# Performance work log

Hardware: AMD Instinct MI355X
Metric: run time of the kernel (lower is better)

The kernel has to match this reference:

```python
import jax, jax.numpy as jnp
import numpy as np

B, L, H = 2, 2048, 1024
NH = 4
K = int(H * 0.5)       # key_dim = 512
V = int(H * 1.0)       # value_dim = 1024
DK, DV = K // NH, V // NH   # 128, 256
PR = 32                # proj_low_rank_dim
GR = 64                # gate_low_rank_dim
EPS = 1e-5


def setup_inputs() -> dict:
    key = jax.random.key(0)
    ks = jax.random.split(key, 16)
    s = 0.02
    return {
        "x": jax.random.normal(ks[0], (B, L, H), jnp.float32),
        "mu_x": jax.random.normal(ks[1], (H,), jnp.float32) * s,      # LerpLinear mu of x_proj[0]
        "Wx1": jax.random.normal(ks[2], (5 * PR, H), jnp.float32) * s,  # x_proj[0].linear
        "Wx2": jax.random.normal(ks[3], (H, 5 * PR), jnp.float32) * s,  # x_proj[2]
        "x_bias": jax.random.normal(ks[4], (5, H), jnp.float32) * s,
        "Wr": jax.random.normal(ks[5], (K, H), jnp.float32) * s,
        "Wk": jax.random.normal(ks[6], (K, H), jnp.float32) * s,
        "Wv": jax.random.normal(ks[7], (V, H), jnp.float32) * s,
        "Wg": jax.random.normal(ks[8], (V, H), jnp.float32) * s,
        "Ww1": jax.random.normal(ks[9], (GR, H), jnp.float32) * s,     # w_proj LoRA down
        "Ww2": jax.random.normal(ks[10], (K, GR), jnp.float32) * s,    # w_proj LoRA up
        "bw2": jax.random.normal(ks[11], (K,), jnp.float32) * s,
        "bonus": jax.random.normal(ks[12], (NH, DK), jnp.float32) * s,  # u
        "ln_w": jnp.ones((DV,), jnp.float32),
        "ln_b": jnp.zeros((DV,), jnp.float32),
        "Wo": jax.random.normal(ks[13], (H, V), jnp.float32) * s,
    }


def reference(x, mu_x, Wx1, Wx2, x_bias, Wr, Wk, Wv, Wg, Ww1, Ww2, bw2,
              bonus, ln_w, ln_b, Wo):
    b, l, h = x.shape
    # token shift: shifted[t] = x[t-1], zeros at t=0 (nn.ZeroPad2d((0,0,1,-1)))
    shifted = jnp.pad(x, ((0, 0), (1, 0), (0, 0)))[:, :-1]
    delta = shifted - x

    # x_proj: LerpLinear -> tanh -> einsum with o_proj-like weight, 5 mixing vectors
    xp = jnp.tanh((x + delta * mu_x) @ Wx1.T).reshape(b, l, 5, PR)
    mus = jnp.einsum('blnr,hnr->blnh', xp, Wx2.reshape(H, 5, PR)) + x_bias
    mu_r, mu_w, mu_k, mu_v, mu_g = (mus[:, :, i] for i in range(5))

    # DDLerpLinear projections: linear(x + delta * mu)
    r = (x + delta * mu_r) @ Wr.T                                   # [B,L,K]
    w = jnp.tanh((x + delta * mu_w) @ Ww1.T) @ Ww2.T + bw2          # LoRA, [B,L,K]
    k = (x + delta * mu_k) @ Wk.T                                   # [B,L,K]
    v = (x + delta * mu_v) @ Wv.T                                   # [B,L,V]
    g = (x + delta * mu_g) @ Wg.T                                   # [B,L,V]

    r = r.reshape(b, l, NH, DK)
    k = k.reshape(b, l, NH, DK)
    v = v.reshape(b, l, NH, DV)
    w = -jnp.exp(w.reshape(b, l, NH, DK))   # log-decay (negative)

    def step(S, inp):
        r_t, k_t, v_t, w_t = inp                                    # [B,h,dk]/[B,h,dv]
        kv = k_t[..., :, None] * v_t[..., None, :]                  # [B,h,dk,dv]
        o_t = jnp.einsum('bhk,bhkv->bhv', r_t,
                         S + bonus[None, :, :, None] * kv)
        S = jnp.exp(w_t)[..., None] * S + kv
        return S, o_t

    seq = (r.transpose(1, 0, 2, 3), k.transpose(1, 0, 2, 3),
           v.transpose(1, 0, 2, 3), w.transpose(1, 0, 2, 3))
    S0 = jnp.zeros((b, NH, DK, DV), x.dtype)
    _, o = jax.lax.scan(step, S0, seq)       # [L,B,h,dv]
    o = o.transpose(1, 0, 2, 3)              # [B,L,h,dv]

    # per-head LayerNorm fused with swish gate
    mean = o.mean(-1, keepdims=True)
    var = o.var(-1, keepdims=True)
    o = (o - mean) * jax.lax.rsqrt(var + EPS) * ln_w + ln_b
    gh = g.reshape(b, l, NH, DV)
    o = o * (gh * jax.nn.sigmoid(gh))        # swish gate

    return o.reshape(b, l, V) @ Wo.T         # [B,L,H]
```

## Files before the change

kernel.cpp:

```cpp
#include <hip/hip_runtime.h>
#include <cstdint>
#include <cstddef>

#define H     1024
#define LSEQ  2048
#define NHH   4
#define DKK   128
#define DVV   256
#define KDIM  512
#define VDIM  1024
#define GRR   64
#define MTOT  4096

enum { EPI_NONE = 0, EPI_TANH = 1, EPI_DEC = 3 };

typedef __attribute__((ext_vector_type(8))) _Float16 half8;
typedef __attribute__((ext_vector_type(4))) float f32x4;
typedef __attribute__((ext_vector_type(2))) float f32x2;

static __device__ __forceinline__ unsigned short f2h(float f) {
    _Float16 h = (_Float16)f;
    union { _Float16 h; unsigned short u; } c;
    c.h = h;
    return c.u;
}

static __device__ __forceinline__ f32x2 pk_fma(f32x2 a, f32x2 b, f32x2 c) {
    return __builtin_elementwise_fma(a, b, c);
}
static __device__ __forceinline__ f32x2 bcast2(float s) {
    f32x2 r; r.x = s; r.y = s; return r;
}

template<int CTRL>
static __device__ __forceinline__ f32x2 dpp_add2(f32x2 x) {
    int lo = __builtin_amdgcn_update_dpp(0, __float_as_int(x.x), CTRL, 0xf, 0xf, true);
    int hi = __builtin_amdgcn_update_dpp(0, __float_as_int(x.y), CTRL, 0xf, 0xf, true);
    f32x2 m;
    m.x = __int_as_float(lo);
    m.y = __int_as_float(hi);
    return x + m;
}

__global__ __launch_bounds__(256) void lerp5_kernel(
    const float* __restrict__ xp,
    const float* __restrict__ Wx2,
    const float* __restrict__ xb,
    const float* __restrict__ x,
    unsigned short* __restrict__ insb)
{
    __shared__ float As[16][64];
    __shared__ float Bs[16][64];
    const int m0 = blockIdx.x * 64;
    const int n0 = blockIdx.y * 64;
    const int t  = threadIdx.x;
    const int tx = t & 15, ty = t >> 4;
    const int sm = t >> 2;
    const int sq = (t & 3) * 4;
    const int nbase = n0 + tx * 4;

    float4 xv[4], pv[4];
#pragma unroll
    for (int i = 0; i < 4; i++) {
        const int m = m0 + ty * 4 + i;
        xv[i] = *(const float4*)(x + (size_t)m * H + nbase);
        pv[i] = make_float4(0.f, 0.f, 0.f, 0.f);
        if ((m & (LSEQ - 1)) != 0)
            pv[i] = *(const float4*)(x + (size_t)(m - 1) * H + nbase);
    }

    for (int z = 0; z < 5; z++) {
        const int acol = z * 32;
        float acc[4][4];
#pragma unroll
        for (int i = 0; i < 4; i++)
#pragma unroll
            for (int j = 0; j < 4; j++) acc[i][j] = 0.f;

#pragma unroll
        for (int k0 = 0; k0 < 32; k0 += 16) {
            {
                const int m = m0 + sm;
                const float4 av = *(const float4*)(xp + (size_t)m * 256 + acol + k0 + sq);
                As[sq + 0][sm] = av.x; As[sq + 1][sm] = av.y;
                As[sq + 2][sm] = av.z; As[sq + 3][sm] = av.w;
            }
            {
                const int n = n0 + sm;
                const float4 bv = *(const float4*)(Wx2 + (size_t)n * 160 + acol + k0 + sq);
                Bs[sq + 0][sm] = bv.x; Bs[sq + 1][sm] = bv.y;
                Bs[sq + 2][sm] = bv.z; Bs[sq + 3][sm] = bv.w;
            }
            __syncthreads();
#pragma unroll
            for (int kk = 0; kk < 16; kk++) {
                const float4 a = *(const float4*)&As[kk][ty * 4];
                const float4 b = *(const float4*)&Bs[kk][tx * 4];
                const float av2[4] = {a.x, a.y, a.z, a.w};
                const float bv2[4] = {b.x, b.y, b.z, b.w};
#pragma unroll
                for (int i = 0; i < 4; i++)
#pragma unroll
                    for (int j = 0; j < 4; j++) acc[i][j] += av2[i] * bv2[j];
            }
            __syncthreads();
        }

        const float4 bb = *(const float4*)(xb + z * H + nbase);
        unsigned short* dst = insb + (size_t)z * 4194304;
#pragma unroll
        for (int i = 0; i < 4; i++) {
            const int m = m0 + ty * 4 + i;
            float4 r;
            r.x = xv[i].x + (pv[i].x - xv[i].x) * (acc[i][0] + bb.x);
            r.y = xv[i].y + (pv[i].y - xv[i].y) * (acc[i][1] + bb.y);
            r.z = xv[i].z + (pv[i].z - xv[i].z) * (acc[i][2] + bb.z);
            r.w = xv[i].w + (pv[i].w - xv[i].w) * (acc[i][3] + bb.w);
            ushort4 p;
            p.x = f2h(r.x); p.y = f2h(r.y); p.z = f2h(r.z); p.w = f2h(r.w);
            *(ushort4*)(dst + (size_t)m * H + nbase) = p;
        }
    }
}

template<int EPI>
__global__ __launch_bounds__(256) void gemm_mfma_bt(
    const unsigned short* __restrict__ A,
    const unsigned short* __restrict__ A2, int nsplit, int lda,
    const unsigned short* __restrict__ B, int ldb,
    float* __restrict__ C, unsigned short* __restrict__ Ch, int ldc, int K,
    const float* __restrict__ bias)
{
    __shared__ __align__(16) unsigned short As[128 * 32];
    __shared__ __align__(16) unsigned short Bs[128 * 32];
    const int t    = threadIdx.x;
    const int w    = t >> 6;
    const int lane = t & 63;
    const int m0 = blockIdx.x * 128;
    const int n0 = blockIdx.y * 128;
    const unsigned short* Au = (n0 < nsplit) ? A : A2;
    const int mw = (w & 1) * 64;
    const int nw = (w >> 1) * 64;
    const int l15 = lane & 15;
    const int q4  = lane >> 4;

    f32x4 acc[4][4];
#pragma unroll
    for (int i = 0; i < 4; i++)
#pragma unroll
        for (int j = 0; j < 4; j++) {
            f32x4 z = {0.f, 0.f, 0.f, 0.f};
            acc[i][j] = z;
        }

    for (int k0 = 0; k0 < K; k0 += 32) {
        __syncthreads();
#pragma unroll
        for (int jj = 0; jj < 2; jj++) {
            const int c   = w * 128 + jj * 64 + lane;
            const int row = c >> 2;
            const int col = (c & 3) * 8;
            __builtin_amdgcn_global_load_lds(
                (const __attribute__((address_space(1))) void*)(Au + (size_t)(m0 + row) * lda + k0 + col),
                (__attribute__((address_space(3))) void*)((char*)As + (w * 128 + jj * 64) * 16),
                16, 0, 0);
            __builtin_amdgcn_global_load_lds(
                (const __attribute__((address_space(1))) void*)(B + (size_t)(n0 + row) * ldb + k0 + col),
                (__attribute__((address_space(3))) void*)((char*)Bs + (w * 128 + jj * 64) * 16),
                16, 0, 0);
        }
        __syncthreads();

        half8 a[4], b[4];
#pragma unroll
        for (int i = 0; i < 4; i++)
            a[i] = *(const half8*)(As + (mw + i * 16 + l15) * 32 + q4 * 8);
#pragma unroll
        for (int j = 0; j < 4; j++)
            b[j] = *(const half8*)(Bs + (nw + j * 16 + l15) * 32 + q4 * 8);
#pragma unroll
        for (int i = 0; i < 4; i++)
#pragma unroll
            for (int j = 0; j < 4; j++)
                acc[i][j] = __builtin_amdgcn_mfma_f32_16x16x32_f16(a[i], b[j], acc[i][j], 0, 0, 0);
    }

#pragma unroll
    for (int i = 0; i < 4; i++) {
        const int m_base = m0 + mw + i * 16 + q4 * 4;
#pragma unroll
        for (int j = 0; j < 4; j++) {
            const int n = n0 + nw + j * 16 + l15;
#pragma unroll
            for (int r = 0; r < 4; r++) {
                float val = acc[i][j][r];
                if constexpr (EPI == EPI_TANH) {
                    C[(size_t)(m_base + r) * ldc + n] = tanhf(val);
                } else if constexpr (EPI == EPI_DEC) {
                    C[(size_t)(m_base + r) * ldc + n] = expf(-expf(val + bias[n]));
                } else {
                    C[(size_t)(m_base + r) * ldc + n] = val;
                }
            }
        }
    }
}

__global__ __launch_bounds__(256) void gemm_fused3(
    const unsigned short* __restrict__ s0, const unsigned short* __restrict__ s1,
    const unsigned short* __restrict__ s2, const unsigned short* __restrict__ s3,
    const unsigned short* __restrict__ s4,
    const unsigned short* __restrict__ Ww1p, const unsigned short* __restrict__ Wrb,
    const unsigned short* __restrict__ Wvb,
    unsigned short* __restrict__ wlow16, float* __restrict__ rkB,
    float* __restrict__ vgB)
{
    const int y = blockIdx.y;
    const unsigned short *Au, *Bp;
    float* C = nullptr;
    unsigned short* Ch = nullptr;
    int n0, ldc;
    if (y == 0) {
        Au = s1; Bp = Ww1p; n0 = 0; ldc = 128; Ch = wlow16;
    } else if (y <= 8) {
        n0 = (y - 1) * 128;
        Au = (n0 < 512) ? s0 : s2;
        Bp = Wrb; C = rkB; ldc = 1024;
    } else {
        n0 = (y - 9) * 128;
        Au = (n0 < 1024) ? s3 : s4;
        Bp = Wvb; C = vgB; ldc = 2048;
    }

    __shared__ __align__(16) unsigned short As[128 * 32];
    __shared__ __align__(16) unsigned short Bs[128 * 32];
    const int t    = threadIdx.x;
    const int w    = t >> 6;
    const int lane = t & 63;
    const int m0 = blockIdx.x * 128;
    const int mw = (w & 1) * 64;
    const int nw = (w >> 1) * 64;
    const int l15 = lane & 15;
    const int q4  = lane >> 4;

    f32x4 acc[4][4];
#pragma unroll
    for (int i = 0; i < 4; i++)
#pragma unroll
        for (int j = 0; j < 4; j++) {
            f32x4 z = {0.f, 0.f, 0.f, 0.f};
            acc[i][j] = z;
        }

    for (int k0 = 0; k0 < H; k0 += 32) {
        __syncthreads();
#pragma unroll
        for (int jj = 0; jj < 2; jj++) {
            const int c   = w * 128 + jj * 64 + lane;
            const int row = c >> 2;
            const int col = (c & 3) * 8;
            __builtin_amdgcn_global_load_lds(
                (const __attribute__((address_space(1))) void*)(Au + (size_t)(m0 + row) * H + k0 + col),
                (__attribute__((address_space(3))) void*)((char*)As + (w * 128 + jj * 64) * 16),
                16, 0, 0);
            __builtin_amdgcn_global_load_lds(
                (const __attribute__((address_space(1))) void*)(Bp + (size_t)(n0 + row) * H + k0 + col),
                (__attribute__((address_space(3))) void*)((char*)Bs + (w * 128 + jj * 64) * 16),
                16, 0, 0);
        }
        __syncthreads();

        half8 a[4], b[4];
#pragma unroll
        for (int i = 0; i < 4; i++)
            a[i] = *(const half8*)(As + (mw + i * 16 + l15) * 32 + q4 * 8);
#pragma unroll
        for (int j = 0; j < 4; j++)
            b[j] = *(const half8*)(Bs + (nw + j * 16 + l15) * 32 + q4 * 8);
#pragma unroll
        for (int i = 0; i < 4; i++)
#pragma unroll
            for (int j = 0; j < 4; j++)
                acc[i][j] = __builtin_amdgcn_mfma_f32_16x16x32_f16(a[i], b[j], acc[i][j], 0, 0, 0);
    }

#pragma unroll
    for (int i = 0; i < 4; i++) {
        const int m_base = m0 + mw + i * 16 + q4 * 4;
#pragma unroll
        for (int j = 0; j < 4; j++) {
            const int n = n0 + nw + j * 16 + l15;
#pragma unroll
            for (int r = 0; r < 4; r++) {
                float val = acc[i][j][r];
                if (Ch) Ch[(size_t)(m_base + r) * ldc + n] = f2h(tanhf(val));
                else    C[(size_t)(m_base + r) * ldc + n] = val;
            }
        }
    }
}

__global__ __launch_bounds__(256) void gemm_mfma_corr(
    const unsigned short* __restrict__ rt16,
    const unsigned short* __restrict__ SentryT16,
    float* __restrict__ o, int segl)
{
    const int z   = blockIdx.z;
    const int seg = (z >> 3) + 1;
    const int bh  = z & 7;
    const int b   = bh >> 2, h = bh & 3;
    const unsigned short* A = rt16 + ((size_t)b * LSEQ + (size_t)seg * segl) * KDIM + h * DKK;
    const unsigned short* B = SentryT16 + (size_t)(seg * 8 + bh) * 32768;
    float* C = o + ((size_t)b * LSEQ + (size_t)seg * segl) * VDIM + h * DVV;

    __shared__ __align__(16) unsigned short As[128 * 32];
    __shared__ __align__(16) unsigned short Bs[128 * 32];
    const int t    = threadIdx.x;
    const int w    = t >> 6;
    const int lane = t & 63;
    const int m0 = blockIdx.x * 128;
    const int n0 = blockIdx.y * 128;
    const int mw = (w & 1) * 64;
    const int nw = (w >> 1) * 64;
    const int l15 = lane & 15;
    const int q4  = lane >> 4;

    f32x4 acc[4][4];
#pragma unroll
    for (int i = 0; i < 4; i++)
#pragma unroll
        for (int j = 0; j < 4; j++) {
            f32x4 zz = {0.f, 0.f, 0.f, 0.f};
            acc[i][j] = zz;
        }

    for (int k0 = 0; k0 < 128; k0 += 32) {
        __syncthreads();
#pragma unroll
        for (int jj = 0; jj < 2; jj++) {
            const int c   = w * 128 + jj * 64 + lane;
            const int row = c >> 2;
            const int col = (c & 3) * 8;
            __builtin_amdgcn_global_load_lds(
                (const __attribute__((address_space(1))) void*)(A + (size_t)(m0 + row) * KDIM + k0 + col),
                (__attribute__((address_space(3))) void*)((char*)As + (w * 128 + jj * 64) * 16),
                16, 0, 0);
            __builtin_amdgcn_global_load_lds(
                (const __attribute__((address_space(1))) void*)(B + (size_t)(n0 + row) * 128 + k0 + col),
                (__attribute__((address_space(3))) void*)((char*)Bs + (w * 128 + jj * 64) * 16),
                16, 0, 0);
        }
        __syncthreads();

        half8 a[4], bb[4];
#pragma unroll
        for (int i = 0; i < 4; i++)
            a[i] = *(const half8*)(As + (mw + i * 16 + l15) * 32 + q4 * 8);
#pragma unroll
        for (int j = 0; j < 4; j++)
            bb[j] = *(const half8*)(Bs + (nw + j * 16 + l15) * 32 + q4 * 8);
#pragma unroll
        for (int i = 0; i < 4; i++)
#pragma unroll
            for (int j = 0; j < 4; j++)
                acc[i][j] = __builtin_amdgcn_mfma_f32_16x16x32_f16(a[i], bb[j], acc[i][j], 0, 0, 0);
    }

#pragma unroll
    for (int i = 0; i < 4; i++) {
        const int mrow = mw + i * 16 + q4 * 4;
        const int m_base = m0 + mrow;
#pragma unroll
        for (int j = 0; j < 4; j++) {
            const int n = n0 + nw + j * 16 + l15;
#pragma unroll
            for (int rr = 0; rr < 4; rr++)
                if (mrow + rr < segl)
                    C[(size_t)(m_base + rr) * VDIM + n] += acc[i][j][rr];
        }
    }
}

__global__ __launch_bounds__(256) void prep_kernel(
    const float* __restrict__ Wr, const float* __restrict__ Wk,
    const float* __restrict__ Wv, const float* __restrict__ Wg,
    const float* __restrict__ Wo, const float* __restrict__ Wx1,
    const float* __restrict__ Ww1, const float* __restrict__ Ww2,
    unsigned short* __restrict__ Wb, unsigned short* __restrict__ Wx1p,
    unsigned short* __restrict__ Ww1p, unsigned short* __restrict__ Ww2p,
    const float* __restrict__ x, const float* __restrict__ mux,
    unsigned short* __restrict__ xl16)
{
    const int bx = blockIdx.x;
    if (bx < 4512) {
        const int q = bx * 256 + threadIdx.x;
        float4 v = make_float4(0.f, 0.f, 0.f, 0.f);
        unsigned short* dst;
        if (q < 1048576) {
            const int i4 = q * 4;
            const float* src; int off;
            if      (i4 <  524288) { src = Wr; off = i4; }
            else if (i4 < 1048576) { src = Wk; off = i4 -  524288; }
            else if (i4 < 2097152) { src = Wv; off = i4 - 1048576; }
            else if (i4 < 3145728) { src = Wg; off = i4 - 2097152; }
            else                   { src = Wo; off = i4 - 3145728; }
            v = *(const float4*)(src + off);
            dst = Wb + i4;
        } else if (q < 1114112) {
            const int e = (q - 1048576) * 4;
            const int row = e >> 10;
            if (row < 160) v = *(const float4*)(Wx1 + (size_t)row * H + (e & 1023));
            dst = Wx1p + e;
        } else if (q < 1146880) {
            const int e = (q - 1114112) * 4;
            const int row = e >> 10;
            if (row < 64) v = *(const float4*)(Ww1 + (size_t)row * H + (e & 1023));
            dst = Ww1p + e;
        } else {
            const int e = (q - 1146880) * 4;
            v = *(const float4*)(Ww2 + e);
            dst = Ww2p + e;
        }
        ushort4 o4;
        o4.x = f2h(v.x); o4.y = f2h(v.y); o4.z = f2h(v.z); o4.w = f2h(v.w);
        *(ushort4*)dst = o4;
    } else {
        const int m = bx - 4512;
        const int c = threadIdx.x * 4;
        const float4 xv = *(const float4*)(x + (size_t)m * H + c);
        float4 pv = make_float4(0.f, 0.f, 0.f, 0.f);
        if ((m & (LSEQ - 1)) != 0)
            pv = *(const float4*)(x + (size_t)(m - 1) * H + c);
        const float4 mv = *(const float4*)(mux + c);
        ushort4 p;
        p.x = f2h(xv.x + (pv.x - xv.x) * mv.x);
        p.y = f2h(xv.y + (pv.y - xv.y) * mv.y);
        p.z = f2h(xv.z + (pv.z - xv.z) * mv.z);
        p.w = f2h(xv.w + (pv.w - xv.w) * mv.w);
        *(ushort4*)(xl16 + (size_t)m * H + c) = p;
    }
}

template<int SEGL_T>
__global__ __launch_bounds__(256, 4) void scan_pass1(
    const float* __restrict__ rk, const float* __restrict__ vg,
    const float* __restrict__ dec, const float* __restrict__ bonus,
    float* __restrict__ o, unsigned short* __restrict__ rt16,
    float* __restrict__ Sloc, float* __restrict__ Dtot)
{
    const int bh  = blockIdx.x & 7;
    const int vc  = (blockIdx.x >> 3) & 7;
    const int seg = blockIdx.x >> 6;
    const int b   = bh >> 2;
    const int h   = bh & 3;
    const int t   = threadIdx.x;
    const int kg  = t & 31;
    const int vl  = t >> 5;
    const bool wlead = (vc == 0) && (vl == 0);

    f32x2 S2[4][2];
    float D[4] = {1.f, 1.f, 1.f, 1.f}, u[4];
#pragma unroll
    for (int j = 0; j < 4; j++) {
        u[j] = bonus[h * DKK + kg * 4 + j];
        f32x2 z = {0.f, 0.f};
        S2[j][0] = z; S2[j][1] = z;
    }

    const size_t row0 = (size_t)b * LSEQ + (size_t)seg * SEGL_T;
    const float* rp = rk  + row0 * 1024 + h * DKK + kg * 4;
    const float* dp = dec + row0 * 512  + h * DKK + kg * 4;
    const float* vp = vg  + row0 * 2048 + h * DVV + vc * 32 + vl * 4;
    float*       op = o   + row0 * 1024 + h * DVV + vc * 32 + vl * 4;
    unsigned short* rt = rt16 + row0 * 512 + h * DKK + kg * 4;

    float4 cr = *(const float4*)rp;
    float4 ck = *(const float4*)(rp + 512);
    float4 cd = *(const float4*)dp;
    float4 cv = *(const float4*)vp;
    rp += 1024; dp += 512; vp += 2048;

#pragma unroll 2
    for (int t0 = 0; t0 < SEGL_T; ++t0) {
        const float4 nr = *(const float4*)rp;
        const float4 nk = *(const float4*)(rp + 512);
        const float4 nd = *(const float4*)dp;
        const float4 nv = *(const float4*)vp;
        rp += 1024; dp += 512; vp += 2048;

        if (wlead) {
            ushort4 p;
            p.x = f2h(cr.x * D[0]); p.y = f2h(cr.y * D[1]);
            p.z = f2h(cr.z * D[2]); p.w = f2h(cr.w * D[3]);
            *(ushort4*)rt = p;
        }
        rt += 512;

        const float ra[4] = {cr.x, cr.y, cr.z, cr.w};
        const float ka[4] = {ck.x, ck.y, ck.z, ck.w};
        const float da[4] = {cd.x, cd.y, cd.z, cd.w};
        f32x2 va2[2];
        va2[0].x = cv.x; va2[0].y = cv.y;
        va2[1].x = cv.z; va2[1].y = cv.w;
        f32x2 part2[2];
        part2[0] = (f32x2){0.f, 0.f};
        part2[1] = (f32x2){0.f, 0.f};
#pragma unroll
        for (int j = 0; j < 4; j++) {
            const f32x2 ka2 = bcast2(ka[j]);
            const f32x2 ra2 = bcast2(ra[j]);
            const f32x2 da2 = bcast2(da[j]);
            const f32x2 u2  = bcast2(u[j]);
#pragma unroll
            for (int p = 0; p < 2; p++) {
                const f32x2 kv2 = va2[p] * ka2;
                const f32x2 su  = pk_fma(u2, kv2, S2[j][p]);
                part2[p]        = pk_fma(ra2, su, part2[p]);
                S2[j][p]        = pk_fma(da2, S2[j][p], kv2);
            }
            D[j] *= da[j];
        }
#pragma unroll
        for (int p = 0; p < 2; p++) {
            part2[p] = dpp_add2<0xB1>(part2[p]);
            part2[p] = dpp_add2<0x4E>(part2[p]);
            part2[p] = dpp_add2<0x141>(part2[p]);
            part2[p] = dpp_add2<0x140>(part2[p]);
            part2[p] = dpp_add2<0x142>(part2[p]);
        }
        if (kg == 31) {
            float4 res = make_float4(part2[0].x, part2[0].y, part2[1].x, part2[1].y);
            *(float4*)op = res;
        }
        op += 1024;
        cr = nr; ck = nk; cd = nd; cv = nv;
    }

    {
        float* sl = Sloc + (size_t)(seg * 8 + bh) * 32768
                    + (size_t)(kg * 4) * 256 + vc * 32 + vl * 4;
#pragma unroll
        for (int j = 0; j < 4; j++) {
            float4 sv = make_float4(S2[j][0].x, S2[j][0].y, S2[j][1].x, S2[j][1].y);
            *(float4*)(sl + j * 256) = sv;
        }
        if (wlead) {
            float* dt = Dtot + (seg * 8 + bh) * 128 + kg * 4;
#pragma unroll
            for (int j = 0; j < 4; j++) dt[j] = D[j];
        }
    }
}

__global__ __launch_bounds__(256) void scan_pass2(
    const float* __restrict__ Sloc, const float* __restrict__ Dtot,
    unsigned short* __restrict__ SentryT16, int nseg)
{
    const int vc = blockIdx.x & 31;
    const int bh = blockIdx.x >> 5;
    const int t  = threadIdx.x;
    const int kg = t & 31;
    const int vl = t >> 5;

    float S[4] = {0.f, 0.f, 0.f, 0.f};
    for (int p = 0; p < nseg; p++) {
        unsigned short* st = SentryT16 + (size_t)(p * 8 + bh) * 32768
                             + (size_t)(vc * 8 + vl) * 128 + kg * 4;
        ushort4 pk;
        pk.x = f2h(S[0]); pk.y = f2h(S[1]); pk.z = f2h(S[2]); pk.w = f2h(S[3]);
        *(ushort4*)st = pk;
        if (p < nseg - 1) {
            const float* sl = Sloc + (size_t)(p * 8 + bh) * 32768
                              + (size_t)(kg * 4) * 256 + vc * 8 + vl;
            const float* dt = Dtot + (p * 8 + bh) * 128 + kg * 4;
#pragma unroll
            for (int j = 0; j < 4; j++) S[j] = dt[j] * S[j] + sl[j * 256];
        }
    }
}

__global__ __launch_bounds__(256) void ln_gate_kernel(
    const float* __restrict__ o, const float* __restrict__ vg,
    const float* __restrict__ lnw, const float* __restrict__ lnb,
    unsigned short* __restrict__ out)
{
    const int m    = blockIdx.x;
    const int t    = threadIdx.x;
    const int h    = t >> 6;
    const int lane = t & 63;
    const size_t obase = (size_t)m * VDIM + (size_t)h * DVV + lane * 4;
    const size_t gbase = (size_t)m * 2048 + 1024 + (size_t)h * DVV + lane * 4;
    const float4 ov = *(const float4*)(o + obase);
    float sum = ov.x + ov.y + ov.z + ov.w;
    float sq  = ov.x * ov.x + ov.y * ov.y + ov.z * ov.z + ov.w * ov.w;
#pragma unroll
    for (int off = 1; off < 64; off <<= 1) {
        sum += __shfl_xor(sum, off);
        sq  += __shfl_xor(sq, off);
    }
    const float mean = sum * (1.f / DVV);
    const float var  = sq * (1.f / DVV) - mean * mean;
    const float rstd = rsqrtf(var + 1e-5f);
    const float4 gv = *(const float4*)(vg + gbase);
    const float4 wv = *(const float4*)(lnw + lane * 4);
    const float4 bv = *(const float4*)(lnb + lane * 4);
    float4 res;
    res.x = ((ov.x - mean) * rstd * wv.x + bv.x) * (gv.x / (1.f + expf(-gv.x)));
    res.y = ((ov.y - mean) * rstd * wv.y + bv.y) * (gv.y / (1.f + expf(-gv.y)));
    res.z = ((ov.z - mean) * rstd * wv.z + bv.z) * (gv.z / (1.f + expf(-gv.z)));
    res.w = ((ov.w - mean) * rstd * wv.w + bv.w) * (gv.w / (1.f + expf(-gv.w)));
    ushort4 p;
    p.x = f2h(res.x); p.y = f2h(res.y); p.z = f2h(res.z); p.w = f2h(res.w);
    *(ushort4*)(out + obase) = p;
}

extern "C" void kernel_launch(void* const* d_in, const int* in_sizes, int n_in,
                              void* d_out, int out_size, void* d_ws, size_t ws_size,
                              hipStream_t stream)
{
    const float* x     = (const float*)d_in[0];
    const float* mu_x  = (const float*)d_in[1];
    const float* Wx1   = (const float*)d_in[2];
    const float* Wx2   = (const float*)d_in[3];
    const float* xb    = (const float*)d_in[4];
    const float* Wr    = (const float*)d_in[5];
    const float* Wk    = (const float*)d_in[6];
    const float* Wv    = (const float*)d_in[7];
    const float* Wg    = (const float*)d_in[8];
    const float* Ww1   = (const float*)d_in[9];
    const float* Ww2   = (const float*)d_in[10];
    const float* bw2   = (const float*)d_in[11];
    const float* bonus = (const float*)d_in[12];
    const float* lnw   = (const float*)d_in[13];
    const float* lnb   = (const float*)d_in[14];
    const float* Wo    = (const float*)d_in[15];
    float* out = (float*)d_out;
    (void)in_sizes; (void)n_in; (void)out_size; (void)ws_size;

    float* ws = (float*)d_ws;
    unsigned short* Wx1p = (unsigned short*)(ws + 0);
    unsigned short* Ww1p = (unsigned short*)(ws + 131072);
    unsigned short* Ww2p = (unsigned short*)(ws + 196608);
    unsigned short* Wb   = (unsigned short*)(ws + 212992);
    float* xp     = ws + 2310144;
    unsigned short* wlow16 = (unsigned short*)(ws + 3358720);
    float* insB   = ws + 3620864;
    float* rkB    = ws + 14106624;
    float* vgB    = ws + 18301952;
    float* decB   = ws + 26692608;

    unsigned short* insb = (unsigned short*)insB;
    unsigned short* Wrb  = Wb;
    unsigned short* Wvb  = Wb + 1048576;
    unsigned short* Wob  = Wb + 3145728;
    unsigned short* xl16 = (unsigned short*)rkB;
    float*          o       = insB;
    unsigned short* rt16    = insb + 2ul * 4194304;
    float*          Sloc    = insB + 3ul * 2097152;
    float*          Dtot    = (float*)wlow16;
    unsigned short* SentryT16 = (unsigned short*)decB;
    unsigned short* gatedb  = (unsigned short*)(insB + 3ul * 2097152);

    const int nseg = 16;
    const int segl = LSEQ / nseg;

    dim3 blk(256);

    prep_kernel<<<dim3(8608), blk, 0, stream>>>(Wr, Wk, Wv, Wg, Wo, Wx1, Ww1, Ww2,
                                                Wb, Wx1p, Ww1p, Ww2p, x, mu_x, xl16);

    gemm_mfma_bt<EPI_TANH><<<dim3(32, 2), blk, 0, stream>>>(
        xl16, xl16, 1 << 30, H, Wx1p, H, xp, nullptr, 256, H, nullptr);

    lerp5_kernel<<<dim3(64, 16), blk, 0, stream>>>(xp, Wx2, xb, x, insb);

    gemm_fused3<<<dim3(32, 25), blk, 0, stream>>>(
        insb + 0ul * 4194304, insb + 1ul * 4194304, insb + 2ul * 4194304,
        insb + 3ul * 4194304, insb + 4ul * 4194304,
        Ww1p, Wrb, Wvb, wlow16, rkB, vgB);

    gemm_mfma_bt<EPI_DEC><<<dim3(32, 4), blk, 0, stream>>>(
        wlow16, wlow16, 1 << 30, 128, Ww2p, 64, decB, nullptr, KDIM, 64, bw2);

    scan_pass1<128><<<dim3(1024), blk, 0, stream>>>(rkB, vgB, decB, bonus,
                                                    o, rt16, Sloc, Dtot);
    scan_pass2<<<dim3(256), blk, 0, stream>>>(Sloc, Dtot, SentryT16, nseg);
    gemm_mfma_corr<<<dim3(1, 2, (nseg - 1) * 8), blk, 0, stream>>>(
        rt16, SentryT16, o, segl);

    ln_gate_kernel<<<dim3(4096), blk, 0, stream>>>(o, vgB, lnw, lnb, gatedb);

    gemm_mfma_bt<EPI_NONE><<<dim3(32, 8), blk, 0, stream>>>(
        gatedb, gatedb, 1 << 30, VDIM, Wob, VDIM, out, nullptr, H, VDIM, nullptr);
}
```

Before: 396.0 us.

## Remap scan_pass1 threads to 16 k-groups of 8 rows by 2 value columns

Changes the thread-to-state mapping in the chunked scan pass: each thread now owns 8 key rows by 2 value columns instead of 4 by 4. The cross-lane reduction over key groups shrinks from 32 lanes to 16, so it needs one fewer DPP step. The packed f32x2 FMAs are replaced by scalar fmaf. The trade-off is that each thread loads twice as much r/k/decay per step and fewer v values, and the stores become narrower float2 writes.

```diff
diff --git a/kernel.cpp b/kernel.cpp
--- a/kernel.cpp
+++ b/kernel.cpp
@@ -23,13 +23,6 @@
     union { _Float16 h; unsigned short u; } c;
     c.h = h;
     return c.u;
-}
-
-static __device__ __forceinline__ f32x2 pk_fma(f32x2 a, f32x2 b, f32x2 c) {
-    return __builtin_elementwise_fma(a, b, c);
-}
-static __device__ __forceinline__ f32x2 bcast2(float s) {
-    f32x2 r; r.x = s; r.y = s; return r;
 }
 
 template<int CTRL>
@@ -454,100 +447,103 @@
     const int b   = bh >> 2;
     const int h   = bh & 3;
     const int t   = threadIdx.x;
-    const int kg  = t & 31;
-    const int vl  = t >> 5;
+    const int kg  = t & 15;
+    const int vl  = t >> 4;
     const bool wlead = (vc == 0) && (vl == 0);
 
-    f32x2 S2[4][2];
-    float D[4] = {1.f, 1.f, 1.f, 1.f}, u[4];
-#pragma unroll
-    for (int j = 0; j < 4; j++) {
-        u[j] = bonus[h * DKK + kg * 4 + j];
-        f32x2 z = {0.f, 0.f};
-        S2[j][0] = z; S2[j][1] = z;
-    }
+    float S0[8], S1[8], D[8], u[8];
+    {
+        const float4 ub0 = *(const float4*)(bonus + h * DKK + kg * 8);
+        const float4 ub1 = *(const float4*)(bonus + h * DKK + kg * 8 + 4);
+        u[0] = ub0.x; u[1] = ub0.y; u[2] = ub0.z; u[3] = ub0.w;
+        u[4] = ub1.x; u[5] = ub1.y; u[6] = ub1.z; u[7] = ub1.w;
+    }
+#pragma unroll
+    for (int j = 0; j < 8; j++) { S0[j] = 0.f; S1[j] = 0.f; D[j] = 1.f; }
 
     const size_t row0 = (size_t)b * LSEQ + (size_t)seg * SEGL_T;
-    const float* rp = rk  + row0 * 1024 + h * DKK + kg * 4;
-    const float* dp = dec + row0 * 512  + h * DKK + kg * 4;
-    const float* vp = vg  + row0 * 2048 + h * DVV + vc * 32 + vl * 4;
-    float*       op = o   + row0 * 1024 + h * DVV + vc * 32 + vl * 4;
-    unsigned short* rt = rt16 + row0 * 512 + h * DKK + kg * 4;
-
-    float4 cr = *(const float4*)rp;
-    float4 ck = *(const float4*)(rp + 512);
-    float4 cd = *(const float4*)dp;
-    float4 cv = *(const float4*)vp;
+    const float* rp = rk  + row0 * 1024 + h * DKK + kg * 8;
+    const float* dp = dec + row0 * 512  + h * DKK + kg * 8;
+    const float* vp = vg  + row0 * 2048 + h * DVV + vc * 32 + vl * 2;
+    float*       op = o   + row0 * 1024 + h * DVV + vc * 32 + vl * 2;
+    unsigned short* rt0 = rt16 + row0 * 512 + h * DKK + kg * 8;
+
+    float4 cr0 = *(const float4*)rp;
+    float4 cr1 = *(const float4*)(rp + 4);
+    float4 ck0 = *(const float4*)(rp + 512);
+    float4 ck1 = *(const float4*)(rp + 516);
+    float4 cd0 = *(const float4*)dp;
+    float4 cd1 = *(const float4*)(dp + 4);
+    float2 cv  = *(const float2*)vp;
     rp += 1024; dp += 512; vp += 2048;
 
 #pragma unroll 2
     for (int t0 = 0; t0 < SEGL_T; ++t0) {
-        const float4 nr = *(const float4*)rp;
-        const float4 nk = *(const float4*)(rp + 512);
-        const float4 nd = *(const float4*)dp;
-        const float4 nv = *(const float4*)vp;
+        const float4 nr0 = *(const float4*)rp;
+        const float4 nr1 = *(const float4*)(rp + 4);
+        const float4 nk0 = *(const float4*)(rp + 512);
+        const float4 nk1 = *(const float4*)(rp + 516);
+        const float4 nd0 = *(const float4*)dp;
+        const float4 nd1 = *(const float4*)(dp + 4);
+        const float2 nv  = *(const float2*)vp;
         rp += 1024; dp += 512; vp += 2048;
 
+        const float ra[8] = {cr0.x, cr0.y, cr0.z, cr0.w, cr1.x, cr1.y, cr1.z, cr1.w};
+        const float ka[8] = {ck0.x, ck0.y, ck0.z, ck0.w, ck1.x, ck1.y, ck1.z, ck1.w};
+        const float da[8] = {cd0.x, cd0.y, cd0.z, cd0.w, cd1.x, cd1.y, cd1.z, cd1.w};
+
         if (wlead) {
-            ushort4 p;
-            p.x = f2h(cr.x * D[0]); p.y = f2h(cr.y * D[1]);
-            p.z = f2h(cr.z * D[2]); p.w = f2h(cr.w * D[3]);
-            *(ushort4*)rt = p;
-        }
-        rt += 512;
-
-        const float ra[4] = {cr.x, cr.y, cr.z, cr.w};
-        const float ka[4] = {ck.x, ck.y, ck.z, ck.w};
-        const float da[4] = {cd.x, cd.y, cd.z, cd.w};
-        f32x2 va2[2];
-        va2[0].x = cv.x; va2[0].y = cv.y;
-        va2[1].x = cv.z; va2[1].y = cv.w;
-        f32x2 part2[2];
-        part2[0] = (f32x2){0.f, 0.f};
-        part2[1] = (f32x2){0.f, 0.f};
-#pragma unroll
-        for (int j = 0; j < 4; j++) {
-            const f32x2 ka2 = bcast2(ka[j]);
-            const f32x2 ra2 = bcast2(ra[j]);
-            const f32x2 da2 = bcast2(da[j]);
-            const f32x2 u2  = bcast2(u[j]);
-#pragma unroll
-            for (int p = 0; p < 2; p++) {
-                const f32x2 kv2 = va2[p] * ka2;
-                const f32x2 su  = pk_fma(u2, kv2, S2[j][p]);
-                part2[p]        = pk_fma(ra2, su, part2[p]);
-                S2[j][p]        = pk_fma(da2, S2[j][p], kv2);
-            }
+            unsigned short* rtp = rt0 + (size_t)t0 * 512;
+            ushort4 p0, p1;
+            p0.x = f2h(ra[0] * D[0]); p0.y = f2h(ra[1] * D[1]);
+            p0.z = f2h(ra[2] * D[2]); p0.w = f2h(ra[3] * D[3]);
+            p1.x = f2h(ra[4] * D[4]); p1.y = f2h(ra[5] * D[5]);
+            p1.z = f2h(ra[6] * D[6]); p1.w = f2h(ra[7] * D[7]);
+            *(ushort4*)rtp       = p0;
+            *(ushort4*)(rtp + 4) = p1;
+        }
+
+        float part0 = 0.f, part1 = 0.f;
+#pragma unroll
+        for (int j = 0; j < 8; j++) {
+            const float kv0 = ka[j] * cv.x;
+            const float kv1 = ka[j] * cv.y;
+            part0 = fmaf(ra[j], fmaf(u[j], kv0, S0[j]), part0);
+            part1 = fmaf(ra[j], fmaf(u[j], kv1, S1[j]), part1);
+            S0[j] = fmaf(da[j], S0[j], kv0);
+            S1[j] = fmaf(da[j], S1[j], kv1);
             D[j] *= da[j];
         }
-#pragma unroll
-        for (int p = 0; p < 2; p++) {
-            part2[p] = dpp_add2<0xB1>(part2[p]);
-            part2[p] = dpp_add2<0x4E>(part2[p]);
-            part2[p] = dpp_add2<0x141>(part2[p]);
-            part2[p] = dpp_add2<0x140>(part2[p]);
-            part2[p] = dpp_add2<0x142>(part2[p]);
-        }
-        if (kg == 31) {
-            float4 res = make_float4(part2[0].x, part2[0].y, part2[1].x, part2[1].y);
-            *(float4*)op = res;
+
+        f32x2 part2; part2.x = part0; part2.y = part1;
+        part2 = dpp_add2<0xB1>(part2);
+        part2 = dpp_add2<0x4E>(part2);
+        part2 = dpp_add2<0x141>(part2);
+        part2 = dpp_add2<0x140>(part2);
+
+        if (kg == 15) {
+            float2 res = make_float2(part2.x, part2.y);
+            *(float2*)op = res;
         }
         op += 1024;
-        cr = nr; ck = nk; cd = nd; cv = nv;
+        cr0 = nr0; cr1 = nr1; ck0 = nk0; ck1 = nk1;
+        cd0 = nd0; cd1 = nd1; cv = nv;
     }
 
     {
         float* sl = Sloc + (size_t)(seg * 8 + bh) * 32768
-                    + (size_t)(kg * 4) * 256 + vc * 32 + vl * 4;
-#pragma unroll
-        for (int j = 0; j < 4; j++) {
-            float4 sv = make_float4(S2[j][0].x, S2[j][0].y, S2[j][1].x, S2[j][1].y);
-            *(float4*)(sl + j * 256) = sv;
+                    + (size_t)(kg * 8) * 256 + vc * 32 + vl * 2;
+#pragma unroll
+        for (int j = 0; j < 8; j++) {
+            float2 sv = make_float2(S0[j], S1[j]);
+            *(float2*)(sl + j * 256) = sv;
         }
         if (wlead) {
-            float* dt = Dtot + (seg * 8 + bh) * 128 + kg * 4;
-#pragma unroll
-            for (int j = 0; j < 4; j++) dt[j] = D[j];
+            float* dt = Dtot + (seg * 8 + bh) * 128 + kg * 8;
+            float4 d0 = make_float4(D[0], D[1], D[2], D[3]);
+            float4 d1 = make_float4(D[4], D[5], D[6], D[7]);
+            *(float4*)dt       = d0;
+            *(float4*)(dt + 4) = d1;
         }
     }
 }
```

After: 516.0 us. 1.3x slower.
